# Optimization experiments

Measured on AMD Instinct MI355X. Metric: run time of the kernel, lower is better.

## Reference

```python
import jax, jax.numpy as jnp
import numpy as np

EPS = 1e-05


def _rms_norm(x, w):
    xf = x.astype(jnp.float32)
    o = xf * jax.lax.rsqrt(jnp.square(xf).mean(-1, keepdims=True) + EPS)
    return (o * w.astype(jnp.float32)).astype(x.dtype)


def _apply_rope(x, sin, cos):
    # x: [B,T,N,H]; sin/cos: [B,T,H/2]
    half = x.shape[-1] // 2
    x1, x2 = x[..., :half], x[..., half:]
    s, c = sin[:, :, None, :], cos[:, :, None, :]
    return jnp.concatenate([x1 * c - x2 * s, x2 * c + x1 * s], axis=-1).astype(x.dtype)


def setup_inputs() -> dict:
    key = jax.random.key(0)
    ks = jax.random.split(key, 12)
    B, T, D, FF, HALF = 2, 1024, 4096, 12288, 64
    return {
        "x": jax.random.normal(ks[0], (B, T, D), jnp.float32),
        "sin": jax.random.uniform(ks[1], (B, T, HALF), jnp.float32),
        "cos": jax.random.uniform(ks[2], (B, T, HALF), jnp.float32),
        "attn_norm_w": jax.random.uniform(ks[3], (D,), jnp.float32),
        "ff_norm_w": jax.random.uniform(ks[4], (D,), jnp.float32),
        "wq": jax.random.normal(ks[5], (D, D), jnp.float32) * 0.02,
        "wk": jax.random.normal(ks[6], (D, D), jnp.float32) * 0.02,
        "wv": jax.random.normal(ks[7], (D, D), jnp.float32) * 0.02,
        "wo": jax.random.normal(ks[8], (D, D), jnp.float32) * 0.02,
        "w_ff": jax.random.normal(ks[9], (D, FF), jnp.float32) * 0.02,
        "w_up": jax.random.normal(ks[10], (D, FF), jnp.float32) * 0.02,
        "w_out": jax.random.normal(ks[11], (FF, D), jnp.float32) * 0.02,
    }


def reference(x, sin, cos, attn_norm_w, ff_norm_w, wq, wk, wv, wo, w_ff, w_up, w_out):
    B, T, D = x.shape
    head_dim = sin.shape[-1] * 2  # 128
    # --- attention ---
    xn = _rms_norm(x, attn_norm_w)
    q = (xn @ wq).reshape(B, T, -1, head_dim)
    k = (xn @ wk).reshape(B, T, -1, head_dim)
    v = (xn @ wv).reshape(B, T, -1, head_dim)
    q = _apply_rope(q, sin, cos)
    k = _apply_rope(k, sin, cos)
    scale = jnp.asarray(1.0 / np.sqrt(head_dim), dtype=q.dtype)
    logits = jnp.einsum("BTNH,BSNH->BNTS", q, k) * scale
    probs = jax.nn.softmax(logits.astype(jnp.float32), axis=-1).astype(k.dtype)
    attn = jnp.einsum("BNTS,BSNH->BTNH", probs, v).reshape(B, T, D)
    x = x + attn @ wo
    # --- SwiGLU MLP ---
    res = x
    xn = _rms_norm(x, ff_norm_w)
    h = jax.nn.silu(xn @ w_ff) * (xn @ w_up)
    return res + h @ w_out
```

## Files before the change

kernel.cpp:

```cpp
#include <hip/hip_runtime.h>
#include <type_traits>


#define D_MODEL 4096
#define FF_DIM  12288
#define SEQ     1024
#define NBATCH  2
#define M_ROWS  2048
#define NHEAD   32
#define HDIM    128
#define QKV_N   12288
#define FF2_N   24576

typedef short bf16x8 __attribute__((ext_vector_type(8)));
typedef ushort u16x16 __attribute__((ext_vector_type(16)));
typedef float f32x4  __attribute__((ext_vector_type(4)));

__device__ __forceinline__ ushort f2bf(float f) {
  unsigned u = __float_as_uint(f);
  u += 0x7FFFu + ((u >> 16) & 1u);
  return (ushort)(u >> 16);
}
__device__ __forceinline__ float bf2f(ushort u) {
  return __uint_as_float(((unsigned)u) << 16);
}

__device__ __forceinline__ void gload_lds16(const ushort* gsrc, ushort* ldst) {
  __builtin_amdgcn_global_load_lds((const __attribute__((address_space(1))) void*)gsrc,
                                   (__attribute__((address_space(3))) void*)ldst, 16, 0, 0);
}

#define SBAR()   asm volatile("s_barrier" ::: "memory")
#define LGKM0()  asm volatile("s_waitcnt lgkmcnt(0)" ::: "memory")
#define VMCNT8() asm volatile("s_waitcnt vmcnt(8)" ::: "memory")

__global__ __launch_bounds__(256)
void transpose_convert(const float* __restrict__ W, ushort* __restrict__ Wt,
                       int K, int N, int remap, int upoff)
{
  __shared__ float tile[64][68];
  const int t = threadIdx.x;
  const size_t k0 = (size_t)blockIdx.y * 64, n0 = (size_t)blockIdx.x * 64;
  const int lx = (t & 15) * 4, ly = t >> 4;
#pragma unroll
  for (int i = 0; i < 64; i += 16)
    *(float4*)&tile[ly + i][lx] = *(const float4*)&W[(k0 + ly + i) * N + n0 + lx];
  __syncthreads();
  const int n = t >> 2, kq = (t & 3) * 16;
  u16x16 ov;
#pragma unroll
  for (int e = 0; e < 16; e++) ov[e] = f2bf(tile[kq + e][n]);
  size_t nOut = n0 + n;
  if (remap) nOut = ((nOut >> 7) << 8) + (nOut & 127) + upoff;
  *(u16x16*)&Wt[nOut * K + k0 + kq] = ov;
}

__global__ __launch_bounds__(256)
void v_transpose(const ushort* __restrict__ v, ushort* __restrict__ vt)
{
  __shared__ ushort tile[32][33];
  const int x = threadIdx.x, y = threadIdx.y;
  const int row0 = blockIdx.x * 32;
  const int d0 = blockIdx.y * 32;
  const int h = blockIdx.z;
  const int b = row0 >> 10, sl0 = row0 & (SEQ - 1);
#pragma unroll
  for (int i = 0; i < 32; i += 8)
    tile[y + i][x] = v[(size_t)(row0 + y + i) * QKV_N + h * HDIM + d0 + x];
  __syncthreads();
  ushort* ob = vt + ((size_t)(b * NHEAD + h) * HDIM + d0) * SEQ + sl0;
#pragma unroll
  for (int i = 0; i < 32; i += 8)
    ob[(size_t)(y + i) * SEQ + x] = tile[x][y + i];
}

__global__ __launch_bounds__(256)
void rmsnorm_kernel(const float* __restrict__ x, const float* __restrict__ w,
                    ushort* __restrict__ out)
{
  const int row = blockIdx.x, t = threadIdx.x;
  const float* xr = x + (size_t)row * D_MODEL;
  float4 vv[4];
  float ss = 0.f;
#pragma unroll
  for (int p = 0; p < 4; p++) {
    vv[p] = *(const float4*)&xr[p * 1024 + t * 4];
    ss += vv[p].x * vv[p].x + vv[p].y * vv[p].y + vv[p].z * vv[p].z + vv[p].w * vv[p].w;
  }
#pragma unroll
  for (int mm = 1; mm < 64; mm <<= 1) ss += __shfl_xor(ss, mm);
  __shared__ float wsum[4];
  if ((t & 63) == 0) wsum[t >> 6] = ss;
  __syncthreads();
  ss = wsum[0] + wsum[1] + wsum[2] + wsum[3];
  const float rs = rsqrtf(ss * (1.f / 4096.f) + 1e-5f);
#pragma unroll
  for (int p = 0; p < 4; p++) {
    const float4 wv = *(const float4*)&w[p * 1024 + t * 4];
    ushort4 ov;
    ov.x = f2bf(vv[p].x * rs * wv.x);
    ov.y = f2bf(vv[p].y * rs * wv.y);
    ov.z = f2bf(vv[p].z * rs * wv.z);
    ov.w = f2bf(vv[p].w * rs * wv.w);
    *(ushort4*)&out[(size_t)row * D_MODEL + p * 1024 + t * 4] = ov;
  }
}

__global__ __launch_bounds__(256)
void rope_kernel(ushort* __restrict__ q, ushort* __restrict__ k,
                 const float* __restrict__ sinp, const float* __restrict__ cosp,
                 int ld)
{
  const size_t idx = (size_t)blockIdx.x * 256 + threadIdx.x;
  const int d = (int)(idx & 63);
  const int h = (int)((idx >> 6) & 31);
  const int t = (int)(idx >> 11);
  const float s = sinp[t * 64 + d], c = cosp[t * 64 + d];
  const size_t base = (size_t)t * ld + h * HDIM + d;
  const float q1 = bf2f(q[base]), q2 = bf2f(q[base + 64]);
  q[base]      = f2bf(q1 * c - q2 * s);
  q[base + 64] = f2bf(q2 * c + q1 * s);
  const float k1 = bf2f(k[base]), k2 = bf2f(k[base + 64]);
  k[base]      = f2bf(k1 * c - k2 * s);
  k[base + 64] = f2bf(k2 * c + k1 * s);
}

__global__ __launch_bounds__(64)
void attn_fwd(const ushort* __restrict__ q, const ushort* __restrict__ k,
              const ushort* __restrict__ vt, ushort* __restrict__ o,
              int ldq, int ldo)
{
  const int l = threadIdx.x, c16 = l & 15, g = l >> 4;
  const int qt = blockIdx.x, h = blockIdx.y, b = blockIdx.z;
  __shared__ __align__(16) ushort P_lds[2][16 * 32];

  const size_t head_off = (size_t)h * HDIM;
  const ushort* vtb = vt + (size_t)(b * NHEAD + h) * HDIM * SEQ;
  bf16x8 qf[2][4];
#pragma unroll
  for (int tile = 0; tile < 2; tile++) {
    const size_t rowQ = (size_t)(b * SEQ + qt * 32 + tile * 16 + c16);
#pragma unroll
    for (int kc = 0; kc < 4; kc++)
      qf[tile][kc] = *(const bf16x8*)(q + rowQ * ldq + head_off + kc * 32 + g * 8);
  }

  f32x4 oacc[2][8];
#pragma unroll
  for (int tile = 0; tile < 2; tile++)
#pragma unroll
    for (int i = 0; i < 8; i++) oacc[tile][i] = (f32x4){0.f, 0.f, 0.f, 0.f};
  float mrow[2][4], lsum[2][4];
#pragma unroll
  for (int tile = 0; tile < 2; tile++)
#pragma unroll
    for (int r = 0; r < 4; r++) { mrow[tile][r] = -1e30f; lsum[tile][r] = 0.f; }
  const float scale = 0.08838834764831845f;
  const float L2E = 1.4426950408889634f;

  for (int s0 = 0; s0 < SEQ; s0 += 32) {
    bf16x8 kfr[2][4];
#pragma unroll
    for (int t = 0; t < 2; t++) {
      const ushort* kb = k + (size_t)(b * SEQ + s0 + t * 16 + c16) * ldq + head_off + g * 8;
#pragma unroll
      for (int kc = 0; kc < 4; kc++) kfr[t][kc] = *(const bf16x8*)(kb + kc * 32);
    }
    f32x4 st[2][2];
#pragma unroll
    for (int tile = 0; tile < 2; tile++)
#pragma unroll
      for (int t = 0; t < 2; t++) {
        f32x4 a = (f32x4){0.f, 0.f, 0.f, 0.f};
#pragma unroll
        for (int kc = 0; kc < 4; kc++)
          a = __builtin_amdgcn_mfma_f32_16x16x32_bf16(qf[tile][kc], kfr[t][kc], a, 0, 0, 0);
        st[tile][t] = a;
      }

    float s0v[2][4], s1v[2][4];
    float worst = -1e30f;
#pragma unroll
    for (int tile = 0; tile < 2; tile++)
#pragma unroll
      for (int r = 0; r < 4; r++) {
        s0v[tile][r] = st[tile][0][r] * scale;
        s1v[tile][r] = st[tile][1][r] * scale;
        worst = fmaxf(worst, fmaxf(s0v[tile][r], s1v[tile][r]) - mrow[tile][r]);
      }

    if (__any(worst > 8.0f)) {
#pragma unroll
      for (int tile = 0; tile < 2; tile++) {
        float a4[4];
#pragma unroll
        for (int r = 0; r < 4; r++) {
          float cm = fmaxf(s0v[tile][r], s1v[tile][r]);
#pragma unroll
          for (int mm = 1; mm < 16; mm <<= 1) cm = fmaxf(cm, __shfl_xor(cm, mm));
          const float mn = fmaxf(mrow[tile][r], cm);
          a4[r] = exp2f((mrow[tile][r] - mn) * L2E);
          mrow[tile][r] = mn;
          const float p0 = exp2f((s0v[tile][r] - mn) * L2E);
          const float p1 = exp2f((s1v[tile][r] - mn) * L2E);
          lsum[tile][r] = lsum[tile][r] * a4[r] + p0 + p1;
          P_lds[tile][(g * 4 + r) * 32 + c16]      = f2bf(p0);
          P_lds[tile][(g * 4 + r) * 32 + 16 + c16] = f2bf(p1);
        }
        const f32x4 av = (f32x4){a4[0], a4[1], a4[2], a4[3]};
#pragma unroll
        for (int dbi = 0; dbi < 8; dbi++) oacc[tile][dbi] *= av;
      }
    } else {
#pragma unroll
      for (int tile = 0; tile < 2; tile++)
#pragma unroll
        for (int r = 0; r < 4; r++) {
          const float p0 = exp2f((s0v[tile][r] - mrow[tile][r]) * L2E);
          const float p1 = exp2f((s1v[tile][r] - mrow[tile][r]) * L2E);
          lsum[tile][r] += p0 + p1;
          P_lds[tile][(g * 4 + r) * 32 + c16]      = f2bf(p0);
          P_lds[tile][(g * 4 + r) * 32 + 16 + c16] = f2bf(p1);
        }
    }
    __syncthreads();
    const bf16x8 pf0 = *(const bf16x8*)&P_lds[0][c16 * 32 + g * 8];
    const bf16x8 pf1 = *(const bf16x8*)&P_lds[1][c16 * 32 + g * 8];
#pragma unroll
    for (int dbi = 0; dbi < 8; dbi++) {
      const bf16x8 vf = *(const bf16x8*)(vtb + (size_t)(dbi * 16 + c16) * SEQ + s0 + g * 8);
      oacc[0][dbi] = __builtin_amdgcn_mfma_f32_16x16x32_bf16(pf0, vf, oacc[0][dbi], 0, 0, 0);
      oacc[1][dbi] = __builtin_amdgcn_mfma_f32_16x16x32_bf16(pf1, vf, oacc[1][dbi], 0, 0, 0);
    }
    __syncthreads();
  }

#pragma unroll
  for (int tile = 0; tile < 2; tile++)
#pragma unroll
    for (int r = 0; r < 4; r++) {
#pragma unroll
      for (int mm = 1; mm < 16; mm <<= 1)
        lsum[tile][r] += __shfl_xor(lsum[tile][r], mm);
    }
#pragma unroll
  for (int tile = 0; tile < 2; tile++) {
    const size_t rowO = (size_t)(b * SEQ + qt * 32 + tile * 16 + g * 4);
#pragma unroll
    for (int dbi = 0; dbi < 8; dbi++)
#pragma unroll
      for (int r = 0; r < 4; r++)
        o[(rowO + r) * ldo + head_off + dbi * 16 + c16] =
            f2bf(oacc[tile][dbi][r] / lsum[tile][r]);
  }
}

__global__ __launch_bounds__(256)
void add2bf_kernel(const ushort* __restrict__ p0, const ushort* __restrict__ p1,
                   ushort* __restrict__ g, int n8)
{
  for (int i = blockIdx.x * 256 + threadIdx.x; i < n8; i += gridDim.x * 256) {
    const bf16x8 a = *(const bf16x8*)&p0[(size_t)i * 8];
    const bf16x8 b = *(const bf16x8*)&p1[(size_t)i * 8];
    ushort ov[8];
#pragma unroll
    for (int e = 0; e < 8; e++)
      ov[e] = f2bf(bf2f((ushort)a[e]) + bf2f((ushort)b[e]));
    *(bf16x8*)&g[(size_t)i * 8] = *(bf16x8*)ov;
  }
}

__global__ __launch_bounds__(256)
void add3bf_kernel(const float* __restrict__ a, const ushort* __restrict__ p0,
                   const ushort* __restrict__ p1, float* __restrict__ d, int n8)
{
  for (int i = blockIdx.x * 256 + threadIdx.x; i < n8; i += gridDim.x * 256) {
    const float4 a0 = ((const float4*)a)[i * 2];
    const float4 a1 = ((const float4*)a)[i * 2 + 1];
    const bf16x8 b = *(const bf16x8*)&p0[(size_t)i * 8];
    const bf16x8 c = *(const bf16x8*)&p1[(size_t)i * 8];
    float4 d0, d1;
    d0.x = a0.x + bf2f((ushort)b[0]) + bf2f((ushort)c[0]);
    d0.y = a0.y + bf2f((ushort)b[1]) + bf2f((ushort)c[1]);
    d0.z = a0.z + bf2f((ushort)b[2]) + bf2f((ushort)c[2]);
    d0.w = a0.w + bf2f((ushort)b[3]) + bf2f((ushort)c[3]);
    d1.x = a1.x + bf2f((ushort)b[4]) + bf2f((ushort)c[4]);
    d1.y = a1.y + bf2f((ushort)b[5]) + bf2f((ushort)c[5]);
    d1.z = a1.z + bf2f((ushort)b[6]) + bf2f((ushort)c[6]);
    d1.w = a1.w + bf2f((ushort)b[7]) + bf2f((ushort)c[7]);
    ((float4*)d)[i * 2]     = d0;
    ((float4*)d)[i * 2 + 1] = d1;
  }
}

template <int EPI, bool SPLITK>
__global__ __launch_bounds__(512, 2)
void gemm8p(const ushort* __restrict__ A, const ushort* __restrict__ Bt,
            const float* __restrict__ res, void* __restrict__ Cout,
            int M, int N, int Ks, int ldk, int wps)
{
  __shared__ __align__(16) ushort lds[65536];
  const int tid = threadIdx.x;
  const int w = tid >> 6, l = tid & 63;
  const int c16 = l & 15, g = l >> 4;
  const int wr = w >> 2, wc = w & 3;

  const int nwg = gridDim.x;
  const int q8 = nwg >> 3, r8 = nwg & 7;
  const int xcd = blockIdx.x & 7, loc = blockIdx.x >> 3;
  int wg = (xcd < r8 ? xcd * (q8 + 1) : r8 * (q8 + 1) + (xcd - r8) * q8) + loc;
  int kslice = 0;
  if constexpr (SPLITK) { kslice = wg / wps; wg -= kslice * wps; }
  const size_t m0 = (size_t)(wg & 7) * 256;
  const size_t n0 = (size_t)(wg >> 3) * 256;
  const int nk = Ks >> 6;

  const int srow  = (w << 3) + (l >> 3);
  const int scolE = ((l & 7) ^ (l >> 3)) << 3;
  const ushort* gA = A  + (size_t)kslice * Ks + (m0 + srow) * (size_t)ldk + scolE;
  const ushort* gB = Bt + (size_t)kslice * Ks + (n0 + srow) * (size_t)ldk + scolE;

#define STG_A(p, h, q, tk)                                                        \
  gload_lds16(gA + (size_t)((h) * 128 + (q) * 64) * ldk + (size_t)(tk) * 64,      \
              lds + (p) * 16384 + (h) * 8192 + (q) * 4096 + (w << 9))
#define STG_B(p, h, q, tk)                                                        \
  gload_lds16(gB + (size_t)((h) * 128 + (q) * 64) * ldk + (size_t)(tk) * 64,      \
              lds + 32768 + (p) * 16384 + (h) * 8192 + (q) * 4096 + (w << 9))
#define STG_A2(p, h, tk) do { STG_A(p, h, 0, tk); STG_A(p, h, 1, tk); } while (0)
#define STG_B2(p, h, tk) do { STG_B(p, h, 0, tk); STG_B(p, h, 1, tk); } while (0)

  const int xorE = (c16 & 7) << 3;
  const int k0E = (g * 8) ^ xorE;
  const int k1E = (32 + g * 8) ^ xorE;
  const int aRow = wr * 64 + c16;
  const int bRow = wc * 32 + c16;

  const char* ldsb = (const char*)lds;
  const char* pA0 = ldsb + aRow * 128 + k0E * 2;
  const char* pA1 = ldsb + aRow * 128 + k1E * 2;
  const char* pB0 = ldsb + 65536 + bRow * 128 + k0E * 2;
  const char* pB1 = ldsb + 65536 + bRow * 128 + k1E * 2;

#define RDA(P, qm, i, kk)                                                         \
  (*(const bf16x8*)((kk ? pA1 : pA0) + (P) * 32768 + (qm) * 16384 + (i) * 2048))
#define RDB(P, qn, j, kk)                                                         \
  (*(const bf16x8*)((kk ? pB1 : pB0) + (P) * 32768 + (qn) * 16384 + (j) * 2048))

  f32x4 acc[8][4];
#pragma unroll
  for (int i = 0; i < 8; i++)
#pragma unroll
    for (int j = 0; j < 4; j++) acc[i][j] = (f32x4){0.f, 0.f, 0.f, 0.f};
  bf16x8 a[4][2], b0[2][2], b1[2][2];

  STG_A2(0, 0, 0); STG_A2(0, 1, 0); STG_B2(0, 0, 0); STG_B2(0, 1, 0);
  STG_A2(1, 0, 1); STG_A2(1, 1, 1); STG_B2(1, 0, 1); STG_B2(1, 1, 1);
  VMCNT8(); SBAR();

  auto tileBody = [&](auto Pc, int t) {
    constexpr int P = decltype(Pc)::value;
    const int tn2 = (t + 2 < nk) ? t + 2 : t + 2 - nk;

#pragma unroll
    for (int j = 0; j < 2; ++j) { b0[j][0] = RDB(P, 0, j, 0); b0[j][1] = RDB(P, 0, j, 1); }
#pragma unroll
    for (int i = 0; i < 4; ++i) { a[i][0] = RDA(P, 0, i, 0); a[i][1] = RDA(P, 0, i, 1); }
    LGKM0();
    __builtin_amdgcn_s_setprio(1);
#pragma unroll
    for (int i = 0; i < 4; ++i)
#pragma unroll
      for (int j = 0; j < 2; ++j)
#pragma unroll
        for (int kk = 0; kk < 2; ++kk)
          acc[i][j] = __builtin_amdgcn_mfma_f32_16x16x32_bf16(a[i][kk], b0[j][kk], acc[i][j], 0, 0, 0);
    __builtin_amdgcn_s_setprio(0);
    SBAR();

#pragma unroll
    for (int j = 0; j < 2; ++j) { b1[j][0] = RDB(P, 1, j, 0); b1[j][1] = RDB(P, 1, j, 1); }
    STG_A2(P, 0, tn2);
    STG_B2(P, 0, tn2);
    LGKM0();
    __builtin_amdgcn_s_setprio(1);
#pragma unroll
    for (int i = 0; i < 4; ++i)
#pragma unroll
      for (int j = 0; j < 2; ++j)
#pragma unroll
        for (int kk = 0; kk < 2; ++kk)
          acc[i][2 + j] = __builtin_amdgcn_mfma_f32_16x16x32_bf16(a[i][kk], b1[j][kk], acc[i][2 + j], 0, 0, 0);
    __builtin_amdgcn_s_setprio(0);
    SBAR();

#pragma unroll
    for (int i = 0; i < 4; ++i) { a[i][0] = RDA(P, 1, i, 0); a[i][1] = RDA(P, 1, i, 1); }
    STG_B2(P, 1, tn2);
    LGKM0();
    __builtin_amdgcn_s_setprio(1);
#pragma unroll
    for (int i = 0; i < 4; ++i)
#pragma unroll
      for (int j = 0; j < 2; ++j)
#pragma unroll
        for (int kk = 0; kk < 2; ++kk)
          acc[4 + i][j] = __builtin_amdgcn_mfma_f32_16x16x32_bf16(a[i][kk], b0[j][kk], acc[4 + i][j], 0, 0, 0);
    __builtin_amdgcn_s_setprio(0);
    SBAR();

    STG_A2(P, 1, tn2);
    LGKM0();
    __builtin_amdgcn_s_setprio(1);
#pragma unroll
    for (int i = 0; i < 4; ++i)
#pragma unroll
      for (int j = 0; j < 2; ++j)
#pragma unroll
        for (int kk = 0; kk < 2; ++kk)
          acc[4 + i][2 + j] = __builtin_amdgcn_mfma_f32_16x16x32_bf16(a[i][kk], b1[j][kk], acc[4 + i][2 + j], 0, 0, 0);
    __builtin_amdgcn_s_setprio(0);
    VMCNT8(); SBAR();
  };

  for (int t = 0; t < nk; t += 2) {
    tileBody(std::integral_constant<int, 0>{}, t);
    tileBody(std::integral_constant<int, 1>{}, t + 1);
  }

#pragma unroll
  for (int qm = 0; qm < 2; qm++)
#pragma unroll
    for (int i = 0; i < 4; i++)
#pragma unroll
      for (int qn = 0; qn < 2; qn++)
#pragma unroll
        for (int j = 0; j < 2; j++)
#pragma unroll
          for (int r = 0; r < 4; r++) {
            const size_t row = m0 + qm * 128 + wr * 64 + i * 16 + g * 4 + r;
            if constexpr (EPI == 2) {
              if (qn == 1) continue;
              const float hv = acc[qm * 4 + i][j][r];
              const float uv = acc[qm * 4 + i][2 + j][r];
              const size_t col = (n0 >> 1) + wc * 32 + j * 16 + c16;
              ((ushort*)Cout)[row * (size_t)(N >> 1) + col] =
                  f2bf((hv / (1.f + __expf(-hv))) * uv);
            } else {
              const size_t col = n0 + qn * 128 + wc * 32 + j * 16 + c16;
              const size_t idx = row * N + col;
              const float v = acc[qm * 4 + i][qn * 2 + j][r];
              if constexpr (EPI == 0)      ((ushort*)Cout)[idx] = f2bf(v);
              else if constexpr (EPI == 1) ((float*)Cout)[idx] = res[idx] + v;
              else if constexpr (EPI == 3) ((float*)Cout)[(size_t)kslice * M * N + idx] = v;
              else                         ((ushort*)Cout)[(size_t)kslice * M * N + idx] = f2bf(v);
            }
          }
#undef STG_A
#undef STG_B
#undef STG_A2
#undef STG_B2
#undef RDA
#undef RDB
}

extern "C" void kernel_launch(void* const* d_in, const int* in_sizes, int n_in,
                              void* d_out, int out_size, void* d_ws, size_t ws_size,
                              hipStream_t stream)
{
  const float* x    = (const float*)d_in[0];
  const float* sinp = (const float*)d_in[1];
  const float* cosp = (const float*)d_in[2];
  const float* anw  = (const float*)d_in[3];
  const float* fnw  = (const float*)d_in[4];
  const float* wq   = (const float*)d_in[5];
  const float* wk   = (const float*)d_in[6];
  const float* wv   = (const float*)d_in[7];
  const float* wo   = (const float*)d_in[8];
  const float* wff  = (const float*)d_in[9];
  const float* wup  = (const float*)d_in[10];
  const float* wout = (const float*)d_in[11];
  float* out = (float*)d_out;

  const size_t szDD   = (size_t)D_MODEL * D_MODEL * 2;
  const size_t szDF   = (size_t)D_MODEL * FF_DIM * 2;
  const size_t szAct2 = (size_t)M_ROWS * D_MODEL * 2;
  const size_t szAct4 = (size_t)M_ROWS * D_MODEL * 4;
  const size_t szQKV  = (size_t)M_ROWS * QKV_N * 2;
  const size_t MN     = (size_t)M_ROWS * D_MODEL;
  const size_t MNq    = (size_t)M_ROWS * QKV_N;

  char* ws = (char*)d_ws;
  size_t off = 0;
  auto alloc = [&](size_t bytes) -> char* {
    char* p = ws + off;
    off += (bytes + 255) & ~(size_t)255;
    return p;
  };
  ushort* R1    = (ushort*)alloc(szDF);
  ushort* R2    = (ushort*)alloc(2 * szDF);
  ushort* wot   = (ushort*)alloc(szDD);
  ushort* xn    = (ushort*)alloc(szAct2);
  ushort* qkv   = (ushort*)alloc(szQKV);
  ushort* attnb = (ushort*)alloc(szAct2);
  float*  x2    = (float*)alloc(szAct4);
  ushort* vtb   = (ushort*)alloc(szAct2);
  ushort* partb = (ushort*)alloc(2 * MN * 2);
  if (off > ws_size) return;

  transpose_convert<<<dim3(D_MODEL / 64, D_MODEL / 64), 256, 0, stream>>>(wq, R1, D_MODEL, D_MODEL, 0, 0);
  transpose_convert<<<dim3(D_MODEL / 64, D_MODEL / 64), 256, 0, stream>>>(wk, R1 + (size_t)D_MODEL * D_MODEL, D_MODEL, D_MODEL, 0, 0);
  transpose_convert<<<dim3(D_MODEL / 64, D_MODEL / 64), 256, 0, stream>>>(wv, R1 + 2 * (size_t)D_MODEL * D_MODEL, D_MODEL, D_MODEL, 0, 0);
  transpose_convert<<<dim3(D_MODEL / 64, D_MODEL / 64), 256, 0, stream>>>(wo, wot, D_MODEL, D_MODEL, 0, 0);

  rmsnorm_kernel<<<M_ROWS, 256, 0, stream>>>(x, anw, xn);
  ushort* qpart = R2;
  gemm8p<4, true><<<2 * (M_ROWS / 256) * (QKV_N / 256), 512, 0, stream>>>(
      xn, R1, nullptr, qpart, M_ROWS, QKV_N, D_MODEL / 2, D_MODEL,
      (M_ROWS / 256) * (QKV_N / 256));
  add2bf_kernel<<<2048, 256, 0, stream>>>(qpart, qpart + MNq, qkv, (int)(MNq / 8));

  transpose_convert<<<dim3(FF_DIM / 64, D_MODEL / 64), 256, 0, stream>>>(wff, R2, D_MODEL, FF_DIM, 1, 0);
  transpose_convert<<<dim3(FF_DIM / 64, D_MODEL / 64), 256, 0, stream>>>(wup, R2, D_MODEL, FF_DIM, 1, 128);
  transpose_convert<<<dim3(D_MODEL / 64, FF_DIM / 64), 256, 0, stream>>>(wout, R1, FF_DIM, D_MODEL, 0, 0);

  rope_kernel<<<(M_ROWS * NHEAD * 64) / 256, 256, 0, stream>>>(qkv, qkv + D_MODEL, sinp, cosp, QKV_N);
  v_transpose<<<dim3(M_ROWS / 32, HDIM / 32, NHEAD), dim3(32, 8), 0, stream>>>(qkv + 2 * D_MODEL, vtb);
  attn_fwd<<<dim3(SEQ / 32, NHEAD, NBATCH), 64, 0, stream>>>(qkv, qkv + D_MODEL, vtb, attnb, QKV_N, D_MODEL);
  gemm8p<4, true><<<256, 512, 0, stream>>>(attnb, wot, nullptr, partb, M_ROWS, D_MODEL, D_MODEL / 2, D_MODEL, 128);
  add3bf_kernel<<<2048, 256, 0, stream>>>(x, partb, partb + MN, x2, (int)(MN / 8));

  rmsnorm_kernel<<<M_ROWS, 256, 0, stream>>>(x2, fnw, xn);
  gemm8p<2, false><<<(M_ROWS / 256) * (FF2_N / 256), 512, 0, stream>>>(xn, R2, nullptr, qkv , M_ROWS, FF2_N, D_MODEL, D_MODEL, 0);
  gemm8p<4, true><<<256, 512, 0, stream>>>(qkv, R1, nullptr, partb, M_ROWS, D_MODEL, FF_DIM / 2, FF_DIM, 128);
  add3bf_kernel<<<2048, 256, 0, stream>>>(x2, partb, partb + MN, out, (int)(MN / 8));
}
```

Before: 1.264 ms.

## Fuse split-K reductions into rope/transpose/rmsnorm and retime GEMM A-tile prefetch

The QKV split-K partial sum is folded directly into the RoPE kernel (for Q/K) and the V transpose kernel, removing the separate add2bf pass and its intermediate write. The residual add after the attention output projection is fused with the second RMSNorm in a single kernel that writes both x2 and the normalized bf16 activations. Inside the GEMM main loop, the second A half-tile for the next stage is issued earlier, one barrier is removed and the vmcnt threshold changes, which alters the prefetch pipeline and risks races in LDS double buffering.

```diff
diff --git a/kernel.cpp b/kernel.cpp
--- a/kernel.cpp
+++ b/kernel.cpp
@@ -32,7 +32,7 @@
 
 #define SBAR()   asm volatile("s_barrier" ::: "memory")
 #define LGKM0()  asm volatile("s_waitcnt lgkmcnt(0)" ::: "memory")
-#define VMCNT8() asm volatile("s_waitcnt vmcnt(8)" ::: "memory")
+#define VMCNT6() asm volatile("s_waitcnt vmcnt(6)" ::: "memory")
 
 __global__ __launch_bounds__(256)
 void transpose_convert(const float* __restrict__ W, ushort* __restrict__ Wt,
@@ -56,7 +56,8 @@
 }
 
 __global__ __launch_bounds__(256)
-void v_transpose(const ushort* __restrict__ v, ushort* __restrict__ vt)
+void v_addtrans(const ushort* __restrict__ p0, const ushort* __restrict__ p1,
+                ushort* __restrict__ vt)
 {
   __shared__ ushort tile[32][33];
   const int x = threadIdx.x, y = threadIdx.y;
@@ -65,8 +66,10 @@
   const int h = blockIdx.z;
   const int b = row0 >> 10, sl0 = row0 & (SEQ - 1);
 #pragma unroll
-  for (int i = 0; i < 32; i += 8)
-    tile[y + i][x] = v[(size_t)(row0 + y + i) * QKV_N + h * HDIM + d0 + x];
+  for (int i = 0; i < 32; i += 8) {
+    const size_t idx = (size_t)(row0 + y + i) * QKV_N + 2 * D_MODEL + h * HDIM + d0 + x;
+    tile[y + i][x] = f2bf(bf2f(p0[idx]) + bf2f(p1[idx]));
+  }
   __syncthreads();
   ushort* ob = vt + ((size_t)(b * NHEAD + h) * HDIM + d0) * SEQ + sl0;
 #pragma unroll
@@ -107,22 +110,77 @@
 }
 
 __global__ __launch_bounds__(256)
-void rope_kernel(ushort* __restrict__ q, ushort* __restrict__ k,
-                 const float* __restrict__ sinp, const float* __restrict__ cosp,
-                 int ld)
+void rms_fuse(const float* __restrict__ x, const ushort* __restrict__ p0,
+              const ushort* __restrict__ p1, const float* __restrict__ w,
+              float* __restrict__ x2, ushort* __restrict__ xn)
+{
+  const int row = blockIdx.x, t = threadIdx.x;
+  const size_t rb = (size_t)row * D_MODEL;
+  float s[2][8];
+  float ss = 0.f;
+#pragma unroll
+  for (int c = 0; c < 2; c++) {
+    const int base = c * 2048 + t * 8;
+    const float4 xa = *(const float4*)&x[rb + base];
+    const float4 xb = *(const float4*)&x[rb + base + 4];
+    const bf16x8 a = *(const bf16x8*)&p0[rb + base];
+    const bf16x8 b = *(const bf16x8*)&p1[rb + base];
+    s[c][0] = xa.x + bf2f((ushort)a[0]) + bf2f((ushort)b[0]);
+    s[c][1] = xa.y + bf2f((ushort)a[1]) + bf2f((ushort)b[1]);
+    s[c][2] = xa.z + bf2f((ushort)a[2]) + bf2f((ushort)b[2]);
+    s[c][3] = xa.w + bf2f((ushort)a[3]) + bf2f((ushort)b[3]);
+    s[c][4] = xb.x + bf2f((ushort)a[4]) + bf2f((ushort)b[4]);
+    s[c][5] = xb.y + bf2f((ushort)a[5]) + bf2f((ushort)b[5]);
+    s[c][6] = xb.z + bf2f((ushort)a[6]) + bf2f((ushort)b[6]);
+    s[c][7] = xb.w + bf2f((ushort)a[7]) + bf2f((ushort)b[7]);
+    float4 o0 = {s[c][0], s[c][1], s[c][2], s[c][3]};
+    float4 o1 = {s[c][4], s[c][5], s[c][6], s[c][7]};
+    *(float4*)&x2[rb + base] = o0;
+    *(float4*)&x2[rb + base + 4] = o1;
+#pragma unroll
+    for (int e = 0; e < 8; e++) ss += s[c][e] * s[c][e];
+  }
+#pragma unroll
+  for (int mm = 1; mm < 64; mm <<= 1) ss += __shfl_xor(ss, mm);
+  __shared__ float wsum[4];
+  if ((t & 63) == 0) wsum[t >> 6] = ss;
+  __syncthreads();
+  ss = wsum[0] + wsum[1] + wsum[2] + wsum[3];
+  const float rs = rsqrtf(ss * (1.f / 4096.f) + 1e-5f);
+#pragma unroll
+  for (int c = 0; c < 2; c++) {
+    const int base = c * 2048 + t * 8;
+    const float4 wa = *(const float4*)&w[base];
+    const float4 wb = *(const float4*)&w[base + 4];
+    ushort ov[8];
+    ov[0] = f2bf(s[c][0] * rs * wa.x); ov[1] = f2bf(s[c][1] * rs * wa.y);
+    ov[2] = f2bf(s[c][2] * rs * wa.z); ov[3] = f2bf(s[c][3] * rs * wa.w);
+    ov[4] = f2bf(s[c][4] * rs * wb.x); ov[5] = f2bf(s[c][5] * rs * wb.y);
+    ov[6] = f2bf(s[c][6] * rs * wb.z); ov[7] = f2bf(s[c][7] * rs * wb.w);
+    *(bf16x8*)&xn[rb + base] = *(bf16x8*)ov;
+  }
+}
+
+__global__ __launch_bounds__(256)
+void qk_addrope(const ushort* __restrict__ p0, const ushort* __restrict__ p1,
+                ushort* __restrict__ qkv,
+                const float* __restrict__ sinp, const float* __restrict__ cosp)
 {
   const size_t idx = (size_t)blockIdx.x * 256 + threadIdx.x;
   const int d = (int)(idx & 63);
   const int h = (int)((idx >> 6) & 31);
   const int t = (int)(idx >> 11);
   const float s = sinp[t * 64 + d], c = cosp[t * 64 + d];
-  const size_t base = (size_t)t * ld + h * HDIM + d;
-  const float q1 = bf2f(q[base]), q2 = bf2f(q[base + 64]);
-  q[base]      = f2bf(q1 * c - q2 * s);
-  q[base + 64] = f2bf(q2 * c + q1 * s);
-  const float k1 = bf2f(k[base]), k2 = bf2f(k[base + 64]);
-  k[base]      = f2bf(k1 * c - k2 * s);
-  k[base + 64] = f2bf(k2 * c + k1 * s);
+  const size_t qb = (size_t)t * QKV_N + h * HDIM + d;
+  const size_t kb = qb + D_MODEL;
+  const float q1 = bf2f(p0[qb])      + bf2f(p1[qb]);
+  const float q2 = bf2f(p0[qb + 64]) + bf2f(p1[qb + 64]);
+  qkv[qb]      = f2bf(q1 * c - q2 * s);
+  qkv[qb + 64] = f2bf(q2 * c + q1 * s);
+  const float k1 = bf2f(p0[kb])      + bf2f(p1[kb]);
+  const float k2 = bf2f(p0[kb + 64]) + bf2f(p1[kb + 64]);
+  qkv[kb]      = f2bf(k1 * c - k2 * s);
+  qkv[kb + 64] = f2bf(k2 * c + k1 * s);
 }
 
 __global__ __launch_bounds__(64)
@@ -252,21 +310,6 @@
       for (int r = 0; r < 4; r++)
         o[(rowO + r) * ldo + head_off + dbi * 16 + c16] =
             f2bf(oacc[tile][dbi][r] / lsum[tile][r]);
-  }
-}
-
-__global__ __launch_bounds__(256)
-void add2bf_kernel(const ushort* __restrict__ p0, const ushort* __restrict__ p1,
-                   ushort* __restrict__ g, int n8)
-{
-  for (int i = blockIdx.x * 256 + threadIdx.x; i < n8; i += gridDim.x * 256) {
-    const bf16x8 a = *(const bf16x8*)&p0[(size_t)i * 8];
-    const bf16x8 b = *(const bf16x8*)&p1[(size_t)i * 8];
-    ushort ov[8];
-#pragma unroll
-    for (int e = 0; e < 8; e++)
-      ov[e] = f2bf(bf2f((ushort)a[e]) + bf2f((ushort)b[e]));
-    *(bf16x8*)&g[(size_t)i * 8] = *(bf16x8*)ov;
   }
 }
 
@@ -354,17 +397,19 @@
   bf16x8 a[4][2], b0[2][2], b1[2][2];
 
   STG_A2(0, 0, 0); STG_A2(0, 1, 0); STG_B2(0, 0, 0); STG_B2(0, 1, 0);
-  STG_A2(1, 0, 1); STG_A2(1, 1, 1); STG_B2(1, 0, 1); STG_B2(1, 1, 1);
-  VMCNT8(); SBAR();
+  STG_A2(1, 0, 1); STG_B2(1, 0, 1); STG_B2(1, 1, 1);
+  VMCNT6(); SBAR();
 
   auto tileBody = [&](auto Pc, int t) {
     constexpr int P = decltype(Pc)::value;
+    const int tn1 = (t + 1 < nk) ? t + 1 : 0;
     const int tn2 = (t + 2 < nk) ? t + 2 : t + 2 - nk;
 
 #pragma unroll
     for (int j = 0; j < 2; ++j) { b0[j][0] = RDB(P, 0, j, 0); b0[j][1] = RDB(P, 0, j, 1); }
 #pragma unroll
     for (int i = 0; i < 4; ++i) { a[i][0] = RDA(P, 0, i, 0); a[i][1] = RDA(P, 0, i, 1); }
+    STG_A2(P ^ 1, 1, tn1);
     LGKM0();
     __builtin_amdgcn_s_setprio(1);
 #pragma unroll
@@ -405,12 +450,6 @@
 #pragma unroll
         for (int kk = 0; kk < 2; ++kk)
           acc[4 + i][j] = __builtin_amdgcn_mfma_f32_16x16x32_bf16(a[i][kk], b0[j][kk], acc[4 + i][j], 0, 0, 0);
-    __builtin_amdgcn_s_setprio(0);
-    SBAR();
-
-    STG_A2(P, 1, tn2);
-    LGKM0();
-    __builtin_amdgcn_s_setprio(1);
 #pragma unroll
     for (int i = 0; i < 4; ++i)
 #pragma unroll
@@ -419,7 +458,7 @@
         for (int kk = 0; kk < 2; ++kk)
           acc[4 + i][2 + j] = __builtin_amdgcn_mfma_f32_16x16x32_bf16(a[i][kk], b1[j][kk], acc[4 + i][2 + j], 0, 0, 0);
     __builtin_amdgcn_s_setprio(0);
-    VMCNT8(); SBAR();
+    VMCNT6(); SBAR();
   };
 
   for (int t = 0; t < nk; t += 2) {
@@ -451,7 +490,6 @@
               const float v = acc[qm * 4 + i][qn * 2 + j][r];
               if constexpr (EPI == 0)      ((ushort*)Cout)[idx] = f2bf(v);
               else if constexpr (EPI == 1) ((float*)Cout)[idx] = res[idx] + v;
-              else if constexpr (EPI == 3) ((float*)Cout)[(size_t)kslice * M * N + idx] = v;
               else                         ((ushort*)Cout)[(size_t)kslice * M * N + idx] = f2bf(v);
             }
           }
@@ -517,19 +555,17 @@
   gemm8p<4, true><<<2 * (M_ROWS / 256) * (QKV_N / 256), 512, 0, stream>>>(
       xn, R1, nullptr, qpart, M_ROWS, QKV_N, D_MODEL / 2, D_MODEL,
       (M_ROWS / 256) * (QKV_N / 256));
-  add2bf_kernel<<<2048, 256, 0, stream>>>(qpart, qpart + MNq, qkv, (int)(MNq / 8));
+  qk_addrope<<<(M_ROWS * NHEAD * 64) / 256, 256, 0, stream>>>(qpart, qpart + MNq, qkv, sinp, cosp);
+  v_addtrans<<<dim3(M_ROWS / 32, HDIM / 32, NHEAD), dim3(32, 8), 0, stream>>>(qpart, qpart + MNq, vtb);
 
   transpose_convert<<<dim3(FF_DIM / 64, D_MODEL / 64), 256, 0, stream>>>(wff, R2, D_MODEL, FF_DIM, 1, 0);
   transpose_convert<<<dim3(FF_DIM / 64, D_MODEL / 64), 256, 0, stream>>>(wup, R2, D_MODEL, FF_DIM, 1, 128);
   transpose_convert<<<dim3(D_MODEL / 64, FF_DIM / 64), 256, 0, stream>>>(wout, R1, FF_DIM, D_MODEL, 0, 0);
 
-  rope_kernel<<<(M_ROWS * NHEAD * 64) / 256, 256, 0, stream>>>(qkv, qkv + D_MODEL, sinp, cosp, QKV_N);
-  v_transpose<<<dim3(M_ROWS / 32, HDIM / 32, NHEAD), dim3(32, 8), 0, stream>>>(qkv + 2 * D_MODEL, vtb);
   attn_fwd<<<dim3(SEQ / 32, NHEAD, NBATCH), 64, 0, stream>>>(qkv, qkv + D_MODEL, vtb, attnb, QKV_N, D_MODEL);
   gemm8p<4, true><<<256, 512, 0, stream>>>(attnb, wot, nullptr, partb, M_ROWS, D_MODEL, D_MODEL / 2, D_MODEL, 128);
-  add3bf_kernel<<<2048, 256, 0, stream>>>(x, partb, partb + MN, x2, (int)(MN / 8));
-
-  rmsnorm_kernel<<<M_ROWS, 256, 0, stream>>>(x2, fnw, xn);
+  rms_fuse<<<M_ROWS, 256, 0, stream>>>(x, partb, partb + MN, fnw, x2, xn);
+
   gemm8p<2, false><<<(M_ROWS / 256) * (FF2_N / 256), 512, 0, stream>>>(xn, R2, nullptr, qkv , M_ROWS, FF2_N, D_MODEL, D_MODEL, 0);
   gemm8p<4, true><<<256, 512, 0, stream>>>(qkv, R1, nullptr, partb, M_ROWS, D_MODEL, FF_DIM / 2, FF_DIM, 128);
   add3bf_kernel<<<2048, 256, 0, stream>>>(x2, partb, partb + MN, out, (int)(MN / 8));
```

After: 1.264 ms. Within noise of the previous version (+0.0%).
